# Kernel optimization log

Hardware: AMD Instinct MI355X
Metric: run time of the kernel (lower is better)

Reference implementation:

```python
import jax, jax.numpy as jnp
import numpy as np

N, C, B, HF, WF, HID = 200000, 128, 4, 116, 200, 64
STRIDE = 8
MAX_BEV_RANGE = 72.0
LN_EPS = 1e-5


def setup_inputs() -> dict:
    key = jax.random.key(0)
    ks = jax.random.split(key, 20)
    s = 0.05  # weight scale
    x = jax.random.normal(ks[0], (N, C), jnp.float32)
    # sparse voxel indices: (batch, z, y, x) on a 128x128x5 stride-8 grid
    bi = jax.random.randint(ks[1], (N, 1), 0, B)
    zi = jax.random.randint(ks[2], (N, 1), 0, 5)
    yi = jax.random.randint(ks[3], (N, 1), 0, 128)
    xi = jax.random.randint(ks[4], (N, 1), 0, 128)
    indices = jnp.concatenate([bi, zi, yi, xi], axis=1).astype(jnp.int32)
    voxel_size = jnp.array([0.1, 0.1, 0.2], jnp.float32)
    pc_range = jnp.array([-51.2, -51.2, -5.0, 51.2, 51.2, 3.0], jnp.float32)
    # plausible lidar->image projection: cam_x=-y, cam_y=-z, cam_z=x, K=[1000,800;1000,450]
    Rt = np.array([[0.0, -1.0, 0.0, 0.0],
                   [0.0, 0.0, -1.0, 1.6],
                   [1.0, 0.0, 0.0, 0.0]], np.float32)
    K = np.array([[1000.0, 0.0, 800.0], [0.0, 1000.0, 450.0], [0.0, 0.0, 1.0]], np.float32)
    P = K @ Rt  # [3,4]
    trans = jnp.asarray(np.tile(P[None], (B, 1, 1)))
    trans = trans + 0.01 * jax.random.normal(ks[5], (B, 3, 4), jnp.float32)
    img_feats = jax.random.normal(ks[6], (B, C, HF, WF), jnp.float32)
    return {
        'x': x, 'indices': indices, 'voxel_size': voxel_size, 'pc_range': pc_range,
        'trans_lidar_to_img': trans, 'img_feats': img_feats, 'img_h': 928, 'img_w': 1600,
        'fg_w1': s * jax.random.normal(ks[7], (C, HID)), 'fg_b1': jnp.zeros((HID,)),
        'fg_w2': s * jax.random.normal(ks[8], (HID, 1)), 'fg_b2': jnp.zeros((1,)),
        'rt_w1': s * jax.random.normal(ks[9], (C + 3, HID)), 'rt_b1': jnp.zeros((HID,)),
        'rt_w2': s * jax.random.normal(ks[10], (HID, 3)),
        'rt_b2': jnp.array([2.0, 0.0, -1.0], jnp.float32),
        'le_w1': s * jax.random.normal(ks[11], (2 * C, C)), 'le_b1': jnp.zeros((C,)),
        'le_w2': s * jax.random.normal(ks[12], (C, C)), 'le_b2': jnp.zeros((C,)),
        'ln_g': jnp.ones((C,)), 'ln_b': jnp.zeros((C,)),
    }


def _bilinear_sample(img_t, b, u_norm, v_norm):
    # img_t: [B,H,W,C]; grid_sample bilinear, align_corners=True, padding_mode='zeros'
    Hf, Wf = img_t.shape[1], img_t.shape[2]
    px = (u_norm + 1.0) * 0.5 * (Wf - 1)
    py = (v_norm + 1.0) * 0.5 * (Hf - 1)
    x0 = jnp.floor(px)
    y0 = jnp.floor(py)
    fx, fy = px - x0, py - y0
    x0i, y0i = x0.astype(jnp.int32), y0.astype(jnp.int32)
    out = jnp.zeros((px.shape[0], img_t.shape[-1]), img_t.dtype)
    for dy in (0, 1):
        for dx in (0, 1):
            xi, yi = x0i + dx, y0i + dy
            w = (fx if dx else 1.0 - fx) * (fy if dy else 1.0 - fy)
            inb = (xi >= 0) & (xi < Wf) & (yi >= 0) & (yi < Hf)
            f = img_t[b, jnp.clip(yi, 0, Hf - 1), jnp.clip(xi, 0, Wf - 1)]
            out = out + f * (w * inb.astype(w.dtype))[:, None]
    return out


def _layernorm(h, g, b):
    mu = jnp.mean(h, axis=-1, keepdims=True)
    var = jnp.mean(jnp.square(h - mu), axis=-1, keepdims=True)
    return (h - mu) * jax.lax.rsqrt(var + LN_EPS) * g + b


def reference(x, indices, voxel_size, pc_range, trans_lidar_to_img, img_feats,
              img_h, img_w, fg_w1, fg_b1, fg_w2, fg_b2, rt_w1, rt_b1, rt_w2, rt_b2,
              le_w1, le_b1, le_w2, le_b2, ln_g, ln_b):
    # voxel centers: indices[:,1:]=(z,y,x) -> (x,y,z)
    spatial = indices[:, 1:][:, ::-1].astype(jnp.float32)
    cvs = voxel_size * STRIDE
    centers = spatial * cvs + pc_range[:3] + cvs / 2.0  # [N,3]
    range_norm = jnp.linalg.norm(centers[:, :2], axis=-1, keepdims=True)
    range_norm = jnp.clip(range_norm / max(MAX_BEV_RANGE, 1e-6), 0.0, 1.0)

    # project to image plane
    ones = jnp.ones((centers.shape[0], 1), centers.dtype)
    xyz_hom = jnp.concatenate([centers, ones], axis=1)  # [N,4]
    batch_ids = indices[:, 0]
    P = trans_lidar_to_img[batch_ids]  # [N,3,4]
    pts = jnp.einsum('nij,nj->ni', P, xyz_hom)
    depth = pts[:, 2]
    safe = jnp.maximum(depth, 1e-5)
    u_feat = pts[:, 0] / safe * (float(WF) / float(img_w))
    v_feat = pts[:, 1] / safe * (float(HF) / float(img_h))
    u_norm = 2.0 * (u_feat / max(WF - 1, 1)) - 1.0
    v_norm = 2.0 * (v_feat / max(HF - 1, 1)) - 1.0
    valid = (depth > 1e-5) & (jnp.abs(u_norm) <= 1.0) & (jnp.abs(v_norm) <= 1.0)
    valid_f = valid.astype(jnp.float32)[:, None]  # [N,1]

    # router
    p_fg = jax.nn.sigmoid(jax.nn.relu(x @ fg_w1 + fg_b1) @ fg_w2 + fg_b2)  # [N,1]
    rin = jnp.concatenate([x, range_norm, p_fg, valid_f], axis=-1)
    route_weights = jax.nn.softmax(jax.nn.relu(rin @ rt_w1 + rt_b1) @ rt_w2 + rt_b2, axis=-1)

    # per-point grid_sample gather from image features
    img_t = jnp.transpose(img_feats, (0, 2, 3, 1))  # [B,H,W,C]
    sampled = _bilinear_sample(img_t, batch_ids, u_norm, v_norm)  # [N,C]

    # light fusion expert
    h = jnp.concatenate([x, sampled], axis=-1)
    delta_light = (jax.nn.relu(h @ le_w1 + le_b1) @ le_w2 + le_b2) * valid_f
    delta = route_weights[:, 1:2] * delta_light  # rectified expert disabled (RECTIFY_RATIO=0)

    fusion_gain = jnp.linalg.norm(delta, axis=-1, keepdims=True) / (
        jnp.linalg.norm(x, axis=-1, keepdims=True) + 1e-6)
    fusion_gain = jnp.clip(1.0 - jnp.exp(-fusion_gain), 0.0, 1.0)

    fused = _layernorm(x + delta, ln_g, ln_b)  # [N,C]

    zeros1 = jnp.zeros_like(p_fg)
    quality = jnp.clip(jnp.concatenate(
        [route_weights, p_fg, range_norm, valid_f, zeros1, fusion_gain,
         zeros1, zeros1, zeros1], axis=-1), 0.0, 1.0)  # [N,11]
    return fused, quality
```

## Files before the change

kernel.cpp:

```cpp
#include <hip/hip_runtime.h>

namespace {

typedef __attribute__((ext_vector_type(8))) short bf16x8;
typedef __attribute__((ext_vector_type(4))) float f32x4;

constexpr int C     = 128;
constexpr int HF    = 116;
constexpr int WF    = 200;
constexpr int PTILE = 32;
constexpr int BLK   = 256;
constexpr int NPTS  = 200000;
constexpr int AS_STRIDE  = 264;
constexpr int HID_STRIDE = 136;

constexpr int W_LE1 = 0;
constexpr int W_LE2 = 32768;
constexpr int W_FG  = 49152;
constexpr int W_RT  = 57344;
constexpr size_t IMG_BYTE_OFF = 131072;

constexpr int IMG_BLOCKS = 4 * HF * 2;
constexpr int WP_BLOCKS  = 256;

__device__ __forceinline__ float b2f(unsigned short u) {
  union { unsigned int i; float f; } v; v.i = ((unsigned int)u) << 16; return v.f;
}
__device__ __forceinline__ unsigned short f2b(float f) {
  union { float f; unsigned int i; } v; v.f = f;
  unsigned int i = v.i;
  return (unsigned short)((i + 0x7fffu + ((i >> 16) & 1u)) >> 16);
}
__device__ __forceinline__ void unp(unsigned int u, float& lo, float& hi) {
  union { unsigned int i; float f; } a, b;
  a.i = u << 16; b.i = u & 0xffff0000u; lo = a.f; hi = b.f;
}
__device__ __forceinline__ unsigned int packb(float a, float b) {
  return (unsigned int)f2b(a) | ((unsigned int)f2b(b) << 16);
}

__global__ __launch_bounds__(BLK) void prep_kernel(
    const float* __restrict__ imgf,
    const float* __restrict__ le_w1, const float* __restrict__ le_w2,
    const float* __restrict__ fg_w1, const float* __restrict__ rt_w1,
    short* __restrict__ wpack, short* __restrict__ imgT) {
  __shared__ short buf[100 * HID_STRIDE];
  const int blk = blockIdx.x;
  if (blk < IMG_BLOCKS) {
    const int half = blk & 1, by = blk >> 1;
    const int b = by / HF, y = by - b * HF;
    const int x0 = half * 100;
    const float* s = imgf + (size_t)b * C * HF * WF + (size_t)y * WF + x0;
    for (int i = threadIdx.x; i < C * 25; i += BLK) {
      int c = i / 25, qx = i - c * 25;
      float4 v = *(const float4*)(s + (size_t)c * (HF * WF) + qx * 4);
      int xb = qx * 4;
      buf[(xb + 0) * HID_STRIDE + c] = (short)f2b(v.x);
      buf[(xb + 1) * HID_STRIDE + c] = (short)f2b(v.y);
      buf[(xb + 2) * HID_STRIDE + c] = (short)f2b(v.z);
      buf[(xb + 3) * HID_STRIDE + c] = (short)f2b(v.w);
    }
    __syncthreads();
    short* d = imgT + ((size_t)(b * HF + y) * WF + x0) * C;
    for (int i = threadIdx.x; i < 100 * 16; i += BLK) {
      int xx = i >> 4, c8 = (i & 15) << 3;
      *(uint4*)(d + (size_t)xx * C + c8) = *(const uint4*)&buf[xx * HID_STRIDE + c8];
    }
  } else {
    int idx = (blk - IMG_BLOCKS) * BLK + threadIdx.x;
    if (idx < 32768) {
      int k = idx >> 7, n = idx & 127;
      wpack[W_LE1 + (((k >> 3) * 128 + n) << 3) + (k & 7)] = (short)f2b(le_w1[idx]);
    } else if (idx < 49152) {
      int l = idx - 32768; int k = l >> 7, n = l & 127;
      wpack[W_LE2 + (((k >> 3) * 128 + n) << 3) + (k & 7)] = (short)f2b(le_w2[l]);
    } else if (idx < 57344) {
      int l = idx - 49152; int k = l >> 6, n = l & 63;
      wpack[W_FG + (((k >> 3) * 64 + n) << 3) + (k & 7)] = (short)f2b(fg_w1[l]);
    } else {
      int l = idx - 57344; int k = l >> 6, n = l & 63;
      wpack[W_RT + (((k >> 3) * 64 + n) << 3) + (k & 7)] = (short)f2b(rt_w1[k * 64 + n]);
    }
  }
}

__global__ __launch_bounds__(BLK, 8) void fuse_kernel(
    const float* __restrict__ x,
    const int*   __restrict__ indices,
    const float* __restrict__ vox, const float* __restrict__ pcr,
    const float* __restrict__ trans,
    const int* __restrict__ imgh_p, const int* __restrict__ imgw_p,
    const float* __restrict__ fg_b1v, const float* __restrict__ fg_w2v,
    const float* __restrict__ fg_b2v,
    const float* __restrict__ rt_w1f,
    const float* __restrict__ rt_b1v, const float* __restrict__ rt_w2v,
    const float* __restrict__ rt_b2v,
    const float* __restrict__ le_b1v, const float* __restrict__ le_b2v,
    const float* __restrict__ ln_gv, const float* __restrict__ ln_bv,
    const short* __restrict__ wpack,
    const short* __restrict__ imgT,
    float* __restrict__ out_fused, float* __restrict__ out_qual) {
  __shared__ short As[PTILE * AS_STRIDE];
  __shared__ float s_rn[32], s_pfg[32], s_valid[32], s_px[32], s_py[32];
  __shared__ float s_gain[32], s_rv[32];
  __shared__ float s_route[32][3];
  __shared__ int   s_bat[32];
  __shared__ __align__(16) float s_lnpart[4][16][4];

  const int tid  = threadIdx.x;
  const int n0   = blockIdx.x * PTILE;
  const int wave = tid >> 6;
  const int lane = tid & 63;
  const int q    = lane >> 4;
  const int nn   = lane & 15;

  {
    const float4* xsrc = (const float4*)(x + (size_t)n0 * C);
    for (int i = tid; i < PTILE * C / 4; i += BLK) {
      float4 v = xsrc[i];
      int p = i >> 5, c4 = (i & 31) * 4;
      short4 sv = { (short)f2b(v.x), (short)f2b(v.y), (short)f2b(v.z), (short)f2b(v.w) };
      *(short4*)&As[p * AS_STRIDE + c4] = sv;
    }
  }
  if (tid < PTILE) {
    int p = tid;
    int base = (n0 + p) * 4;
    int bi = indices[base + 0], zi = indices[base + 1];
    int yi = indices[base + 2], xi = indices[base + 3];
    float sp[3] = { (float)xi, (float)yi, (float)zi };
    float cen[3];
#pragma unroll
    for (int k = 0; k < 3; ++k) {
      float cvs = vox[k] * 8.0f;
      cen[k] = sp[k] * cvs + pcr[k] + cvs * 0.5f;
    }
    float rn = sqrtf(cen[0] * cen[0] + cen[1] * cen[1]) / 72.0f;
    rn = fminf(fmaxf(rn, 0.0f), 1.0f);
    float pt[3];
#pragma unroll
    for (int r = 0; r < 3; ++r) {
      const float* row = trans + (bi * 3 + r) * 4;
      pt[r] = row[0] * cen[0] + row[1] * cen[1] + row[2] * cen[2] + row[3];
    }
    float depth = pt[2];
    float safe  = fmaxf(depth, 1e-5f);
    float uf = pt[0] / safe * ((float)WF / (float)imgw_p[0]);
    float vf = pt[1] / safe * ((float)HF / (float)imgh_p[0]);
    float un = 2.0f * (uf / (float)(WF - 1)) - 1.0f;
    float vn = 2.0f * (vf / (float)(HF - 1)) - 1.0f;
    bool valid = (depth > 1e-5f) && (fabsf(un) <= 1.0f) && (fabsf(vn) <= 1.0f);
    s_rn[p] = rn;
    s_valid[p] = valid ? 1.0f : 0.0f;
    s_bat[p] = bi;
    s_px[p] = (un + 1.0f) * 0.5f * (float)(WF - 1);
    s_py[p] = (vn + 1.0f) * 0.5f * (float)(HF - 1);
  }
  __syncthreads();

  f32x4 accS[4];
#pragma unroll
  for (int t = 0; t < 4; ++t) accS[t] = (f32x4){0.f, 0.f, 0.f, 0.f};
  if (wave < 2) {
    const int p0 = wave * 16;
    const bf16x8* Bfg = (const bf16x8*)(wpack + W_FG);
    for (int ks = 0; ks < 4; ++ks) {
      bf16x8 a = *(const bf16x8*)&As[(p0 + nn) * AS_STRIDE + ks * 32 + q * 8];
#pragma unroll
      for (int t = 0; t < 4; ++t) {
        bf16x8 b = Bfg[(ks * 4 + q) * 64 + t * 16 + nn];
        accS[t] = __builtin_amdgcn_mfma_f32_16x16x32_bf16(a, b, accS[t], 0, 0, 0);
      }
    }
    float part[4] = {0.f, 0.f, 0.f, 0.f};
#pragma unroll
    for (int t = 0; t < 4; ++t) {
      int col = t * 16 + nn;
      float bias = fg_b1v[col];
      float w2   = fg_w2v[col];
#pragma unroll
      for (int r = 0; r < 4; ++r)
        part[r] += fmaxf(accS[t][r] + bias, 0.f) * w2;
    }
#pragma unroll
    for (int off = 1; off < 16; off <<= 1) {
#pragma unroll
      for (int r = 0; r < 4; ++r) part[r] += __shfl_xor(part[r], off);
    }
    if (nn == 0) {
      float b2 = fg_b2v[0];
#pragma unroll
      for (int r = 0; r < 4; ++r)
        s_pfg[p0 + q * 4 + r] = 1.f / (1.f + expf(-(part[r] + b2)));
    }
  } else {
    const int p0 = (wave - 2) * 16;
    const bf16x8* Brt = (const bf16x8*)(wpack + W_RT);
    for (int ks = 0; ks < 4; ++ks) {
      bf16x8 a = *(const bf16x8*)&As[(p0 + nn) * AS_STRIDE + ks * 32 + q * 8];
#pragma unroll
      for (int t = 0; t < 4; ++t) {
        bf16x8 b = Brt[(ks * 4 + q) * 64 + t * 16 + nn];
        accS[t] = __builtin_amdgcn_mfma_f32_16x16x32_bf16(a, b, accS[t], 0, 0, 0);
      }
    }
  }
  __syncthreads();

  if (wave >= 2) {
    const int p0 = (wave - 2) * 16;
    float lg0[4] = {0,0,0,0}, lg1[4] = {0,0,0,0}, lg2[4] = {0,0,0,0};
#pragma unroll
    for (int t = 0; t < 4; ++t) {
      int col = t * 16 + nn;
      float b1 = rt_b1v[col];
      float wr = rt_w1f[128 * 64 + col];
      float wp = rt_w1f[129 * 64 + col];
      float wv = rt_w1f[130 * 64 + col];
      float w20 = rt_w2v[col * 3 + 0], w21 = rt_w2v[col * 3 + 1], w22 = rt_w2v[col * 3 + 2];
#pragma unroll
      for (int r = 0; r < 4; ++r) {
        int p = p0 + q * 4 + r;
        float h = accS[t][r] + b1 + s_rn[p] * wr + s_pfg[p] * wp + s_valid[p] * wv;
        h = fmaxf(h, 0.f);
        lg0[r] += h * w20; lg1[r] += h * w21; lg2[r] += h * w22;
      }
    }
#pragma unroll
    for (int off = 1; off < 16; off <<= 1) {
#pragma unroll
      for (int r = 0; r < 4; ++r) {
        lg0[r] += __shfl_xor(lg0[r], off);
        lg1[r] += __shfl_xor(lg1[r], off);
        lg2[r] += __shfl_xor(lg2[r], off);
      }
    }
    if (nn == 0) {
      float rb0 = rt_b2v[0], rb1 = rt_b2v[1], rb2 = rt_b2v[2];
#pragma unroll
      for (int r = 0; r < 4; ++r) {
        int p = p0 + q * 4 + r;
        float l0 = lg0[r] + rb0, l1 = lg1[r] + rb1, l2 = lg2[r] + rb2;
        float m = fmaxf(l0, fmaxf(l1, l2));
        float e0 = expf(l0 - m), e1 = expf(l1 - m), e2 = expf(l2 - m);
        float inv = 1.f / (e0 + e1 + e2);
        s_route[p][0] = e0 * inv; s_route[p][1] = e1 * inv; s_route[p][2] = e2 * inv;
        s_rv[p] = e1 * inv * s_valid[p];
      }
    }
  }
  {
    int p = tid >> 3, grp = tid & 7, ch0 = grp * 16;
    float sacc[16];
#pragma unroll
    for (int k = 0; k < 16; ++k) sacc[k] = 0.f;
    if (s_valid[p] > 0.5f) {
      float px = s_px[p], py = s_py[p];
      float x0f = floorf(px), y0f = floorf(py);
      float fx = px - x0f, fy = py - y0f;
      int ix = (int)x0f, iy = (int)y0f;
      int bb = s_bat[p];
#pragma unroll
      for (int dy = 0; dy < 2; ++dy) {
#pragma unroll
        for (int dx = 0; dx < 2; ++dx) {
          int xi = ix + dx, yi = iy + dy;
          if (xi >= 0 && xi < WF && yi >= 0 && yi < HF) {
            float w = (dx ? fx : 1.0f - fx) * (dy ? fy : 1.0f - fy);
            const short* tp = imgT + (((size_t)bb * HF + yi) * WF + xi) * C + ch0;
            uint4 u0 = *(const uint4*)tp;
            uint4 u1 = *(const uint4*)(tp + 8);
            float lo, hi;
            unp(u0.x, lo, hi); sacc[0] += w * lo;  sacc[1] += w * hi;
            unp(u0.y, lo, hi); sacc[2] += w * lo;  sacc[3] += w * hi;
            unp(u0.z, lo, hi); sacc[4] += w * lo;  sacc[5] += w * hi;
            unp(u0.w, lo, hi); sacc[6] += w * lo;  sacc[7] += w * hi;
            unp(u1.x, lo, hi); sacc[8] += w * lo;  sacc[9] += w * hi;
            unp(u1.y, lo, hi); sacc[10] += w * lo; sacc[11] += w * hi;
            unp(u1.z, lo, hi); sacc[12] += w * lo; sacc[13] += w * hi;
            unp(u1.w, lo, hi); sacc[14] += w * lo; sacc[15] += w * hi;
          }
        }
      }
    }
    uint4 o0 = { packb(sacc[0], sacc[1]),  packb(sacc[2], sacc[3]),
                 packb(sacc[4], sacc[5]),  packb(sacc[6], sacc[7]) };
    uint4 o1 = { packb(sacc[8], sacc[9]),  packb(sacc[10], sacc[11]),
                 packb(sacc[12], sacc[13]), packb(sacc[14], sacc[15]) };
    *(uint4*)&As[p * AS_STRIDE + 128 + ch0]     = o0;
    *(uint4*)&As[p * AS_STRIDE + 128 + ch0 + 8] = o1;
  }
  __syncthreads();

  const int pt = wave & 1, cg = wave >> 1;
  const int p0le = pt * 16;
  const bf16x8* Ble1 = (const bf16x8*)(wpack + W_LE1);
  f32x4 acc[4];
#pragma unroll
  for (int t = 0; t < 4; ++t) acc[t] = (f32x4){0.f, 0.f, 0.f, 0.f};
  for (int ks = 0; ks < 8; ++ks) {
    bf16x8 a = *(const bf16x8*)&As[(p0le + nn) * AS_STRIDE + ks * 32 + q * 8];
#pragma unroll
    for (int t = 0; t < 4; ++t) {
      bf16x8 b = Ble1[(ks * 4 + q) * 128 + (cg * 4 + t) * 16 + nn];
      acc[t] = __builtin_amdgcn_mfma_f32_16x16x32_bf16(a, b, acc[t], 0, 0, 0);
    }
  }
  __syncthreads();
#pragma unroll
  for (int t = 0; t < 4; ++t) {
    int col = (cg * 4 + t) * 16 + nn;
    float bias = le_b1v[col];
#pragma unroll
    for (int r = 0; r < 4; ++r)
      As[(p0le + q * 4 + r) * AS_STRIDE + 128 + col] =
          (short)f2b(fmaxf(acc[t][r] + bias, 0.f));
  }
  __syncthreads();

  const bf16x8* Ble2 = (const bf16x8*)(wpack + W_LE2);
  f32x4 acc2[4];
#pragma unroll
  for (int t = 0; t < 4; ++t) acc2[t] = (f32x4){0.f, 0.f, 0.f, 0.f};
  for (int ks = 0; ks < 4; ++ks) {
    bf16x8 a = *(const bf16x8*)&As[(p0le + nn) * AS_STRIDE + 128 + ks * 32 + q * 8];
#pragma unroll
    for (int t = 0; t < 4; ++t) {
      bf16x8 b = Ble2[(ks * 4 + q) * 128 + (cg * 4 + t) * 16 + nn];
      acc2[t] = __builtin_amdgcn_mfma_f32_16x16x32_bf16(a, b, acc2[t], 0, 0, 0);
    }
  }
  float yv[4][4];
  float psum[4] = {0,0,0,0}, psum2[4] = {0,0,0,0}, pd2[4] = {0,0,0,0}, px2[4] = {0,0,0,0};
#pragma unroll
  for (int t = 0; t < 4; ++t) {
    int col = (cg * 4 + t) * 16 + nn;
    float bias = le_b2v[col];
#pragma unroll
    for (int r = 0; r < 4; ++r) {
      int p = p0le + q * 4 + r;
      float d  = (acc2[t][r] + bias) * s_rv[p];
      float xv = b2f((unsigned short)As[p * AS_STRIDE + col]);
      float y  = xv + d;
      yv[t][r] = y;
      psum[r]  += y;       psum2[r] += y * y;
      pd2[r]   += d * d;   px2[r]   += xv * xv;
    }
  }
#pragma unroll
  for (int off = 1; off < 16; off <<= 1) {
#pragma unroll
    for (int r = 0; r < 4; ++r) {
      psum[r]  += __shfl_xor(psum[r], off);
      psum2[r] += __shfl_xor(psum2[r], off);
      pd2[r]   += __shfl_xor(pd2[r], off);
      px2[r]   += __shfl_xor(px2[r], off);
    }
  }
  if (nn == 0) {
#pragma unroll
    for (int r = 0; r < 4; ++r) {
      f32x4 st = { psum[r], psum2[r], pd2[r], px2[r] };
      *(f32x4*)&s_lnpart[wave][q * 4 + r][0] = st;
    }
  }
  __syncthreads();
  {
    float gcol[4], bcol[4];
#pragma unroll
    for (int t = 0; t < 4; ++t) {
      int col = (cg * 4 + t) * 16 + nn;
      gcol[t] = ln_gv[col]; bcol[t] = ln_bv[col];
    }
#pragma unroll
    for (int r = 0; r < 4; ++r) {
      int lr = q * 4 + r;
      int p  = p0le + lr;
      f32x4 oth = *(const f32x4*)&s_lnpart[wave ^ 2][lr][0];
      float sy  = psum[r]  + oth[0];
      float sy2 = psum2[r] + oth[1];
      float sd2 = pd2[r]   + oth[2];
      float sx2 = px2[r]   + oth[3];
      float mu  = sy * (1.f / 128.f);
      float var = sy2 * (1.f / 128.f) - mu * mu;
      float inv = rsqrtf(var + 1e-5f);
      if (wave < 2 && nn == 0) {
        float gain = sqrtf(sd2) / (sqrtf(sx2) + 1e-6f);
        s_gain[p] = fminf(fmaxf(1.f - expf(-gain), 0.f), 1.f);
      }
      float* orow = out_fused + (size_t)(n0 + p) * C;
#pragma unroll
      for (int t = 0; t < 4; ++t) {
        int col = (cg * 4 + t) * 16 + nn;
        orow[col] = (yv[t][r] - mu) * inv * gcol[t] + bcol[t];
      }
    }
  }
  __syncthreads();

  for (int idx = tid; idx < PTILE * 11; idx += BLK) {
    int p2 = idx / 11, k = idx - p2 * 11;
    float v = 0.0f;
    if (k < 3)       v = s_route[p2][k];
    else if (k == 3) v = s_pfg[p2];
    else if (k == 4) v = s_rn[p2];
    else if (k == 5) v = s_valid[p2];
    else if (k == 7) v = s_gain[p2];
    v = fminf(fmaxf(v, 0.0f), 1.0f);
    out_qual[(size_t)(n0 + p2) * 11 + k] = v;
  }
}

}

extern "C" void kernel_launch(void* const* d_in, const int* in_sizes, int n_in,
                              void* d_out, int out_size, void* d_ws, size_t ws_size,
                              hipStream_t stream) {
  const float* x       = (const float*)d_in[0];
  const int*   indices = (const int*)d_in[1];
  const float* vox     = (const float*)d_in[2];
  const float* pcr     = (const float*)d_in[3];
  const float* trans   = (const float*)d_in[4];
  const float* imgf    = (const float*)d_in[5];
  const int*   imgh    = (const int*)d_in[6];
  const int*   imgw    = (const int*)d_in[7];
  const float* fg_w1   = (const float*)d_in[8];
  const float* fg_b1   = (const float*)d_in[9];
  const float* fg_w2   = (const float*)d_in[10];
  const float* fg_b2   = (const float*)d_in[11];
  const float* rt_w1   = (const float*)d_in[12];
  const float* rt_b1   = (const float*)d_in[13];
  const float* rt_w2   = (const float*)d_in[14];
  const float* rt_b2   = (const float*)d_in[15];
  const float* le_w1   = (const float*)d_in[16];
  const float* le_b1   = (const float*)d_in[17];
  const float* le_w2   = (const float*)d_in[18];
  const float* le_b2   = (const float*)d_in[19];
  const float* ln_g    = (const float*)d_in[20];
  const float* ln_b    = (const float*)d_in[21];

  short* wpack = (short*)d_ws;
  short* imgT  = (short*)((char*)d_ws + IMG_BYTE_OFF);

  float* out_fused = (float*)d_out;
  float* out_qual  = out_fused + (size_t)NPTS * C;

  (void)in_sizes; (void)n_in; (void)out_size; (void)ws_size;

  prep_kernel<<<IMG_BLOCKS + WP_BLOCKS, BLK, 0, stream>>>(
      imgf, le_w1, le_w2, fg_w1, rt_w1, wpack, imgT);
  fuse_kernel<<<NPTS / PTILE, BLK, 0, stream>>>(
      x, indices, vox, pcr, trans, imgh, imgw,
      fg_b1, fg_w2, fg_b2,
      rt_w1, rt_b1, rt_w2, rt_b2,
      le_b1, le_b2, ln_g, ln_b,
      wpack, imgT, out_fused, out_qual);
}
```

Baseline: 341.4 us.

## Make each wave own 16 points end-to-end, replacing block barriers with wave barriers

The block-cooperative work split, where waves shared a 32-point tile across fg/route and LE column groups through __syncthreads, is replaced. Each wave now processes its own 16 points through every stage: both fg and route MFMAs, bilinear gather, both LE layers over all 128 columns, and LayerNorm. Per-point data passes through lane shuffles and a per-wave XOR-swizzled LDS buffer. x is read straight from global memory into MFMA fragments and read again for the residual, which removes the LDS staging and cross-wave LN reduction. The cost is more accumulator registers (launch bound lowered to 6), redundant global x reads, and each wave loading the full weight sets.

```diff
diff --git a/kernel.cpp b/kernel.cpp
--- a/kernel.cpp
+++ b/kernel.cpp
@@ -8,10 +8,10 @@
 constexpr int C     = 128;
 constexpr int HF    = 116;
 constexpr int WF    = 200;
-constexpr int PTILE = 32;
 constexpr int BLK   = 256;
 constexpr int NPTS  = 200000;
-constexpr int AS_STRIDE  = 264;
+constexpr int WPTS  = 16;
+constexpr int PTILE = 64;
 constexpr int HID_STRIDE = 136;
 
 constexpr int W_LE1 = 0;
@@ -37,6 +37,12 @@
 }
 __device__ __forceinline__ unsigned int packb(float a, float b) {
   return (unsigned int)f2b(a) | ((unsigned int)f2b(b) << 16);
+}
+
+__device__ __forceinline__ int swz(int row, int col) {
+  int byte = row * 256 + col * 2;
+  byte ^= (row & 7) << 4;
+  return byte >> 1;
 }
 
 __global__ __launch_bounds__(BLK) void prep_kernel(
@@ -84,7 +90,7 @@
   }
 }
 
-__global__ __launch_bounds__(BLK, 8) void fuse_kernel(
+__global__ __launch_bounds__(BLK, 6) void fuse_kernel(
     const float* __restrict__ x,
     const int*   __restrict__ indices,
     const float* __restrict__ vox, const float* __restrict__ pcr,
@@ -100,32 +106,33 @@
     const short* __restrict__ wpack,
     const short* __restrict__ imgT,
     float* __restrict__ out_fused, float* __restrict__ out_qual) {
-  __shared__ short As[PTILE * AS_STRIDE];
-  __shared__ float s_rn[32], s_pfg[32], s_valid[32], s_px[32], s_py[32];
-  __shared__ float s_gain[32], s_rv[32];
-  __shared__ float s_route[32][3];
-  __shared__ int   s_bat[32];
-  __shared__ __align__(16) float s_lnpart[4][16][4];
+  __shared__ short SH[4][WPTS * 128];
+  __shared__ float s_rn[4][WPTS], s_pfg[4][WPTS], s_valid[4][WPTS];
+  __shared__ float s_rv[4][WPTS], s_gain[4][WPTS];
+  __shared__ float s_route[4][WPTS][3];
 
   const int tid  = threadIdx.x;
-  const int n0   = blockIdx.x * PTILE;
   const int wave = tid >> 6;
   const int lane = tid & 63;
   const int q    = lane >> 4;
   const int nn   = lane & 15;
-
-  {
-    const float4* xsrc = (const float4*)(x + (size_t)n0 * C);
-    for (int i = tid; i < PTILE * C / 4; i += BLK) {
-      float4 v = xsrc[i];
-      int p = i >> 5, c4 = (i & 31) * 4;
-      short4 sv = { (short)f2b(v.x), (short)f2b(v.y), (short)f2b(v.z), (short)f2b(v.w) };
-      *(short4*)&As[p * AS_STRIDE + c4] = sv;
-    }
-  }
-  if (tid < PTILE) {
-    int p = tid;
-    int base = (n0 + p) * 4;
+  const int n0w  = blockIdx.x * PTILE + wave * WPTS;
+  short* sh = &SH[wave][0];
+
+  auto loadA = [&](int row, int k0) -> bf16x8 {
+    const float* xr = x + (size_t)(n0w + row) * C + k0;
+    float4 v0 = *(const float4*)xr;
+    float4 v1 = *(const float4*)(xr + 4);
+    union { bf16x8 h; unsigned int u[4]; } o;
+    o.u[0] = packb(v0.x, v0.y); o.u[1] = packb(v0.z, v0.w);
+    o.u[2] = packb(v1.x, v1.y); o.u[3] = packb(v1.z, v1.w);
+    return o.h;
+  };
+
+  float g_px = 0.f, g_py = 0.f, g_valid = 0.f;
+  int   g_bat = 0;
+  if (lane < WPTS) {
+    int base = (n0w + lane) * 4;
     int bi = indices[base + 0], zi = indices[base + 1];
     int yi = indices[base + 2], xi = indices[base + 3];
     float sp[3] = { (float)xi, (float)yi, (float)zi };
@@ -150,28 +157,31 @@
     float un = 2.0f * (uf / (float)(WF - 1)) - 1.0f;
     float vn = 2.0f * (vf / (float)(HF - 1)) - 1.0f;
     bool valid = (depth > 1e-5f) && (fabsf(un) <= 1.0f) && (fabsf(vn) <= 1.0f);
-    s_rn[p] = rn;
-    s_valid[p] = valid ? 1.0f : 0.0f;
-    s_bat[p] = bi;
-    s_px[p] = (un + 1.0f) * 0.5f * (float)(WF - 1);
-    s_py[p] = (vn + 1.0f) * 0.5f * (float)(HF - 1);
-  }
-  __syncthreads();
-
-  f32x4 accS[4];
-#pragma unroll
-  for (int t = 0; t < 4; ++t) accS[t] = (f32x4){0.f, 0.f, 0.f, 0.f};
-  if (wave < 2) {
-    const int p0 = wave * 16;
+    g_valid = valid ? 1.0f : 0.0f;
+    g_bat = bi;
+    g_px = (un + 1.0f) * 0.5f * (float)(WF - 1);
+    g_py = (vn + 1.0f) * 0.5f * (float)(HF - 1);
+    s_rn[wave][lane] = rn;
+    s_valid[wave][lane] = g_valid;
+  }
+  __builtin_amdgcn_wave_barrier();
+
+  f32x4 afg[4], art[4];
+#pragma unroll
+  for (int t = 0; t < 4; ++t) { afg[t] = (f32x4){0,0,0,0}; art[t] = (f32x4){0,0,0,0}; }
+  {
     const bf16x8* Bfg = (const bf16x8*)(wpack + W_FG);
+    const bf16x8* Brt = (const bf16x8*)(wpack + W_RT);
     for (int ks = 0; ks < 4; ++ks) {
-      bf16x8 a = *(const bf16x8*)&As[(p0 + nn) * AS_STRIDE + ks * 32 + q * 8];
+      bf16x8 a = loadA(nn, ks * 32 + q * 8);
 #pragma unroll
       for (int t = 0; t < 4; ++t) {
-        bf16x8 b = Bfg[(ks * 4 + q) * 64 + t * 16 + nn];
-        accS[t] = __builtin_amdgcn_mfma_f32_16x16x32_bf16(a, b, accS[t], 0, 0, 0);
+        afg[t] = __builtin_amdgcn_mfma_f32_16x16x32_bf16(a, Bfg[(ks * 4 + q) * 64 + t * 16 + nn], afg[t], 0, 0, 0);
+        art[t] = __builtin_amdgcn_mfma_f32_16x16x32_bf16(a, Brt[(ks * 4 + q) * 64 + t * 16 + nn], art[t], 0, 0, 0);
       }
     }
+  }
+  {
     float part[4] = {0.f, 0.f, 0.f, 0.f};
 #pragma unroll
     for (int t = 0; t < 4; ++t) {
@@ -180,7 +190,7 @@
       float w2   = fg_w2v[col];
 #pragma unroll
       for (int r = 0; r < 4; ++r)
-        part[r] += fmaxf(accS[t][r] + bias, 0.f) * w2;
+        part[r] += fmaxf(afg[t][r] + bias, 0.f) * w2;
     }
 #pragma unroll
     for (int off = 1; off < 16; off <<= 1) {
@@ -191,24 +201,17 @@
       float b2 = fg_b2v[0];
 #pragma unroll
       for (int r = 0; r < 4; ++r)
-        s_pfg[p0 + q * 4 + r] = 1.f / (1.f + expf(-(part[r] + b2)));
-    }
-  } else {
-    const int p0 = (wave - 2) * 16;
-    const bf16x8* Brt = (const bf16x8*)(wpack + W_RT);
-    for (int ks = 0; ks < 4; ++ks) {
-      bf16x8 a = *(const bf16x8*)&As[(p0 + nn) * AS_STRIDE + ks * 32 + q * 8];
-#pragma unroll
-      for (int t = 0; t < 4; ++t) {
-        bf16x8 b = Brt[(ks * 4 + q) * 64 + t * 16 + nn];
-        accS[t] = __builtin_amdgcn_mfma_f32_16x16x32_bf16(a, b, accS[t], 0, 0, 0);
-      }
-    }
-  }
-  __syncthreads();
-
-  if (wave >= 2) {
-    const int p0 = (wave - 2) * 16;
+        s_pfg[wave][q * 4 + r] = 1.f / (1.f + expf(-(part[r] + b2)));
+    }
+  }
+  __builtin_amdgcn_wave_barrier();
+  {
+    float rnp[4], pfp[4], vdp[4];
+#pragma unroll
+    for (int r = 0; r < 4; ++r) {
+      int p = q * 4 + r;
+      rnp[r] = s_rn[wave][p]; pfp[r] = s_pfg[wave][p]; vdp[r] = s_valid[wave][p];
+    }
     float lg0[4] = {0,0,0,0}, lg1[4] = {0,0,0,0}, lg2[4] = {0,0,0,0};
 #pragma unroll
     for (int t = 0; t < 4; ++t) {
@@ -220,8 +223,7 @@
       float w20 = rt_w2v[col * 3 + 0], w21 = rt_w2v[col * 3 + 1], w22 = rt_w2v[col * 3 + 2];
 #pragma unroll
       for (int r = 0; r < 4; ++r) {
-        int p = p0 + q * 4 + r;
-        float h = accS[t][r] + b1 + s_rn[p] * wr + s_pfg[p] * wp + s_valid[p] * wv;
+        float h = art[t][r] + b1 + rnp[r] * wr + pfp[r] * wp + vdp[r] * wv;
         h = fmaxf(h, 0.f);
         lg0[r] += h * w20; lg1[r] += h * w21; lg2[r] += h * w22;
       }
@@ -239,27 +241,31 @@
       float rb0 = rt_b2v[0], rb1 = rt_b2v[1], rb2 = rt_b2v[2];
 #pragma unroll
       for (int r = 0; r < 4; ++r) {
-        int p = p0 + q * 4 + r;
+        int p = q * 4 + r;
         float l0 = lg0[r] + rb0, l1 = lg1[r] + rb1, l2 = lg2[r] + rb2;
         float m = fmaxf(l0, fmaxf(l1, l2));
         float e0 = expf(l0 - m), e1 = expf(l1 - m), e2 = expf(l2 - m);
         float inv = 1.f / (e0 + e1 + e2);
-        s_route[p][0] = e0 * inv; s_route[p][1] = e1 * inv; s_route[p][2] = e2 * inv;
-        s_rv[p] = e1 * inv * s_valid[p];
+        s_route[wave][p][0] = e0 * inv; s_route[wave][p][1] = e1 * inv; s_route[wave][p][2] = e2 * inv;
+        s_rv[wave][p] = e1 * inv * vdp[r];
       }
     }
   }
-  {
-    int p = tid >> 3, grp = tid & 7, ch0 = grp * 16;
+  __builtin_amdgcn_wave_barrier();
+
+  for (int it = 0; it < 2; ++it) {
+    int p = it * 8 + (lane >> 3), grp = lane & 7, ch0 = grp * 16;
+    float vld = __shfl(g_valid, p);
+    float px  = __shfl(g_px, p);
+    float py  = __shfl(g_py, p);
+    int   bb  = __shfl(g_bat, p);
     float sacc[16];
 #pragma unroll
     for (int k = 0; k < 16; ++k) sacc[k] = 0.f;
-    if (s_valid[p] > 0.5f) {
-      float px = s_px[p], py = s_py[p];
+    if (vld > 0.5f) {
       float x0f = floorf(px), y0f = floorf(py);
       float fx = px - x0f, fy = py - y0f;
       int ix = (int)x0f, iy = (int)y0f;
-      int bb = s_bat[p];
 #pragma unroll
       for (int dy = 0; dy < 2; ++dy) {
 #pragma unroll
@@ -287,64 +293,64 @@
                  packb(sacc[4], sacc[5]),  packb(sacc[6], sacc[7]) };
     uint4 o1 = { packb(sacc[8], sacc[9]),  packb(sacc[10], sacc[11]),
                  packb(sacc[12], sacc[13]), packb(sacc[14], sacc[15]) };
-    *(uint4*)&As[p * AS_STRIDE + 128 + ch0]     = o0;
-    *(uint4*)&As[p * AS_STRIDE + 128 + ch0 + 8] = o1;
-  }
-  __syncthreads();
-
-  const int pt = wave & 1, cg = wave >> 1;
-  const int p0le = pt * 16;
+    *(uint4*)&sh[swz(p, ch0)]     = o0;
+    *(uint4*)&sh[swz(p, ch0 + 8)] = o1;
+  }
+  __builtin_amdgcn_wave_barrier();
+
   const bf16x8* Ble1 = (const bf16x8*)(wpack + W_LE1);
-  f32x4 acc[4];
-#pragma unroll
-  for (int t = 0; t < 4; ++t) acc[t] = (f32x4){0.f, 0.f, 0.f, 0.f};
+  f32x4 accL[8];
+#pragma unroll
+  for (int t = 0; t < 8; ++t) accL[t] = (f32x4){0,0,0,0};
   for (int ks = 0; ks < 8; ++ks) {
-    bf16x8 a = *(const bf16x8*)&As[(p0le + nn) * AS_STRIDE + ks * 32 + q * 8];
-#pragma unroll
-    for (int t = 0; t < 4; ++t) {
-      bf16x8 b = Ble1[(ks * 4 + q) * 128 + (cg * 4 + t) * 16 + nn];
-      acc[t] = __builtin_amdgcn_mfma_f32_16x16x32_bf16(a, b, acc[t], 0, 0, 0);
-    }
-  }
-  __syncthreads();
-#pragma unroll
-  for (int t = 0; t < 4; ++t) {
-    int col = (cg * 4 + t) * 16 + nn;
+    bf16x8 a = (ks < 4) ? loadA(nn, ks * 32 + q * 8)
+                        : *(const bf16x8*)&sh[swz(nn, (ks - 4) * 32 + q * 8)];
+#pragma unroll
+    for (int t = 0; t < 8; ++t)
+      accL[t] = __builtin_amdgcn_mfma_f32_16x16x32_bf16(a, Ble1[(ks * 4 + q) * 128 + t * 16 + nn], accL[t], 0, 0, 0);
+  }
+  __builtin_amdgcn_wave_barrier();
+#pragma unroll
+  for (int t = 0; t < 8; ++t) {
+    int col = t * 16 + nn;
     float bias = le_b1v[col];
 #pragma unroll
     for (int r = 0; r < 4; ++r)
-      As[(p0le + q * 4 + r) * AS_STRIDE + 128 + col] =
-          (short)f2b(fmaxf(acc[t][r] + bias, 0.f));
-  }
-  __syncthreads();
+      sh[swz(q * 4 + r, col)] = (short)f2b(fmaxf(accL[t][r] + bias, 0.f));
+  }
+  __builtin_amdgcn_wave_barrier();
 
   const bf16x8* Ble2 = (const bf16x8*)(wpack + W_LE2);
-  f32x4 acc2[4];
-#pragma unroll
-  for (int t = 0; t < 4; ++t) acc2[t] = (f32x4){0.f, 0.f, 0.f, 0.f};
+  f32x4 acc2[8];
+#pragma unroll
+  for (int t = 0; t < 8; ++t) acc2[t] = (f32x4){0,0,0,0};
   for (int ks = 0; ks < 4; ++ks) {
-    bf16x8 a = *(const bf16x8*)&As[(p0le + nn) * AS_STRIDE + 128 + ks * 32 + q * 8];
-#pragma unroll
-    for (int t = 0; t < 4; ++t) {
-      bf16x8 b = Ble2[(ks * 4 + q) * 128 + (cg * 4 + t) * 16 + nn];
-      acc2[t] = __builtin_amdgcn_mfma_f32_16x16x32_bf16(a, b, acc2[t], 0, 0, 0);
-    }
-  }
-  float yv[4][4];
+    bf16x8 a = *(const bf16x8*)&sh[swz(nn, ks * 32 + q * 8)];
+#pragma unroll
+    for (int t = 0; t < 8; ++t)
+      acc2[t] = __builtin_amdgcn_mfma_f32_16x16x32_bf16(a, Ble2[(ks * 4 + q) * 128 + t * 16 + nn], acc2[t], 0, 0, 0);
+  }
+
+  float rvp[4];
+#pragma unroll
+  for (int r = 0; r < 4; ++r) rvp[r] = s_rv[wave][q * 4 + r];
   float psum[4] = {0,0,0,0}, psum2[4] = {0,0,0,0}, pd2[4] = {0,0,0,0}, px2[4] = {0,0,0,0};
-#pragma unroll
-  for (int t = 0; t < 4; ++t) {
-    int col = (cg * 4 + t) * 16 + nn;
-    float bias = le_b2v[col];
+  unsigned int xp[4][4];
+#pragma unroll
+  for (int tp = 0; tp < 4; ++tp) {
+    int c0 = (2 * tp) * 16 + nn, c1 = c0 + 16;
+    float b0 = le_b2v[c0], b1 = le_b2v[c1];
 #pragma unroll
     for (int r = 0; r < 4; ++r) {
-      int p = p0le + q * 4 + r;
-      float d  = (acc2[t][r] + bias) * s_rv[p];
-      float xv = b2f((unsigned short)As[p * AS_STRIDE + col]);
-      float y  = xv + d;
-      yv[t][r] = y;
-      psum[r]  += y;       psum2[r] += y * y;
-      pd2[r]   += d * d;   px2[r]   += xv * xv;
+      const float* xr = x + (size_t)(n0w + q * 4 + r) * C;
+      unsigned int up = packb(xr[c0], xr[c1]);
+      xp[r][tp] = up;
+      float xv0, xv1; unp(up, xv0, xv1);
+      float d0 = (acc2[2 * tp][r] + b0) * rvp[r];
+      float d1 = (acc2[2 * tp + 1][r] + b1) * rvp[r];
+      float y0 = xv0 + d0, y1 = xv1 + d1;
+      psum[r]  += y0 + y1;        psum2[r] += y0 * y0 + y1 * y1;
+      pd2[r]   += d0 * d0 + d1 * d1;  px2[r] += xv0 * xv0 + xv1 * xv1;
     }
   }
 #pragma unroll
@@ -360,54 +366,39 @@
   if (nn == 0) {
 #pragma unroll
     for (int r = 0; r < 4; ++r) {
-      f32x4 st = { psum[r], psum2[r], pd2[r], px2[r] };
-      *(f32x4*)&s_lnpart[wave][q * 4 + r][0] = st;
-    }
-  }
-  __syncthreads();
-  {
-    float gcol[4], bcol[4];
-#pragma unroll
-    for (int t = 0; t < 4; ++t) {
-      int col = (cg * 4 + t) * 16 + nn;
-      gcol[t] = ln_gv[col]; bcol[t] = ln_bv[col];
-    }
-#pragma unroll
-    for (int r = 0; r < 4; ++r) {
-      int lr = q * 4 + r;
-      int p  = p0le + lr;
-      f32x4 oth = *(const f32x4*)&s_lnpart[wave ^ 2][lr][0];
-      float sy  = psum[r]  + oth[0];
-      float sy2 = psum2[r] + oth[1];
-      float sd2 = pd2[r]   + oth[2];
-      float sx2 = px2[r]   + oth[3];
-      float mu  = sy * (1.f / 128.f);
-      float var = sy2 * (1.f / 128.f) - mu * mu;
-      float inv = rsqrtf(var + 1e-5f);
-      if (wave < 2 && nn == 0) {
-        float gain = sqrtf(sd2) / (sqrtf(sx2) + 1e-6f);
-        s_gain[p] = fminf(fmaxf(1.f - expf(-gain), 0.f), 1.f);
-      }
-      float* orow = out_fused + (size_t)(n0 + p) * C;
-#pragma unroll
-      for (int t = 0; t < 4; ++t) {
-        int col = (cg * 4 + t) * 16 + nn;
-        orow[col] = (yv[t][r] - mu) * inv * gcol[t] + bcol[t];
-      }
-    }
-  }
-  __syncthreads();
-
-  for (int idx = tid; idx < PTILE * 11; idx += BLK) {
-    int p2 = idx / 11, k = idx - p2 * 11;
+      float gain = sqrtf(pd2[r]) / (sqrtf(px2[r]) + 1e-6f);
+      s_gain[wave][q * 4 + r] = fminf(fmaxf(1.f - expf(-gain), 0.f), 1.f);
+    }
+  }
+#pragma unroll
+  for (int r = 0; r < 4; ++r) {
+    int p = q * 4 + r;
+    float mu  = psum[r] * (1.f / 128.f);
+    float var = psum2[r] * (1.f / 128.f) - mu * mu;
+    float inv = rsqrtf(var + 1e-5f);
+    float* orow = out_fused + (size_t)(n0w + p) * C;
+#pragma unroll
+    for (int tp = 0; tp < 4; ++tp) {
+      int c0 = (2 * tp) * 16 + nn, c1 = c0 + 16;
+      float xv0, xv1; unp(xp[r][tp], xv0, xv1);
+      float d0 = (acc2[2 * tp][r] + le_b2v[c0]) * rvp[r];
+      float d1 = (acc2[2 * tp + 1][r] + le_b2v[c1]) * rvp[r];
+      orow[c0] = (xv0 + d0 - mu) * inv * ln_gv[c0] + ln_bv[c0];
+      orow[c1] = (xv1 + d1 - mu) * inv * ln_gv[c1] + ln_bv[c1];
+    }
+  }
+  __builtin_amdgcn_wave_barrier();
+
+  for (int i = lane; i < WPTS * 11; i += 64) {
+    int p2 = i / 11, k = i - p2 * 11;
     float v = 0.0f;
-    if (k < 3)       v = s_route[p2][k];
-    else if (k == 3) v = s_pfg[p2];
-    else if (k == 4) v = s_rn[p2];
-    else if (k == 5) v = s_valid[p2];
-    else if (k == 7) v = s_gain[p2];
+    if (k < 3)       v = s_route[wave][p2][k];
+    else if (k == 3) v = s_pfg[wave][p2];
+    else if (k == 4) v = s_rn[wave][p2];
+    else if (k == 5) v = s_valid[wave][p2];
+    else if (k == 7) v = s_gain[wave][p2];
     v = fminf(fmaxf(v, 0.0f), 1.0f);
-    out_qual[(size_t)(n0 + p2) * 11 + k] = v;
+    out_qual[(size_t)(n0w + p2) * 11 + k] = v;
   }
 }
 
```

After: 490.2 us. +43.6%, slower.
